# Kernel optimization log

Hardware: AMD Instinct MI355X
Metric: run time of the kernel (lower is better)

## Reference

```python
import jax, jax.numpy as jnp
from jax import lax
import numpy as np

ALPHA = 1.0
GAMMA = 1e-6
KBLK = 64  # codebook block size for the L1 NN search scan


def setup_inputs() -> dict:
    key = jax.random.key(0)
    ks = jax.random.split(key, 6)
    B, T, C, F, D, K = 8, 1024, 32, 256, 128, 512
    return {
        "X": jax.random.normal(ks[0], (B, T, C), jnp.float32),
        "H": jax.random.normal(ks[1], (B, D, T), jnp.float32),
        "M": jax.random.normal(ks[2], (D, K), jnp.float32),
        "Hdec": jax.random.normal(ks[3], (B, T, F), jnp.float32),
        "W": jax.random.normal(ks[4], (C, F), jnp.float32) * 0.05,
        "w_d": jax.random.normal(ks[5], (C,), jnp.float32) * 0.05,
    }


def _memory_loss(H, M):
    # H: [B, D, T], M: [D, K]
    Ht = jnp.transpose(H, (0, 2, 1))            # [B, T, D]
    MT = M.T                                     # [K, D] codewords
    K, D = MT.shape
    nblk = K // KBLK
    blocks = MT.reshape(nblk, KBLK, D)
    bases = jnp.arange(nblk, dtype=jnp.int32) * KBLK

    def step(carry, blk_base):
        best_d, best_i = carry
        blk, base = blk_base
        # L1 distance to this block of codewords: [B, T, KBLK]
        d = jnp.sum(jnp.abs(Ht[:, :, None, :] - blk[None, None, :, :]), axis=-1)
        bd = jnp.min(d, axis=-1)
        bi = jnp.argmin(d, axis=-1).astype(jnp.int32) + base
        upd = bd < best_d  # strict < keeps the first (lowest-index) argmin, as torch does
        return (jnp.where(upd, bd, best_d), jnp.where(upd, bi, best_i)), None

    init = (jnp.full(Ht.shape[:2], jnp.inf, Ht.dtype),
            jnp.zeros(Ht.shape[:2], jnp.int32))
    (_, best_i), _ = lax.scan(step, init, (blocks, bases))

    Zt = MT[best_i]  # [B, T, D] gathered nearest codewords
    sg = lax.stop_gradient
    # sum of per-(b,d) squared L2 norms over T == total squared sum
    diffs = jnp.sum((sg(Ht) - Zt) ** 2) + jnp.sum((Ht - sg(Zt)) ** 2)
    return diffs / float(np.prod(H.shape))


def reference(X, H, M, Hdec, W, w_d):
    # decoder last layer + discriminator head (needed for adaptive weight grads)
    def rec_loss(w):
        Xhat = jnp.einsum('btf,cf->btc', Hdec, w)
        return jnp.mean((Xhat - X) ** 2)

    def d_loss(w):
        Xhat = jnp.einsum('btf,cf->btc', Hdec, w)
        return -jnp.mean(Xhat @ w_d)

    loss_rec = rec_loss(W)
    loss_d = d_loss(W)
    loss_m = _memory_loss(H, M)

    g_rec = jax.grad(rec_loss)(W)
    g_d = jax.grad(d_loss)(W)
    lmbda = lax.stop_gradient(
        jnp.linalg.norm(g_rec) / (jnp.linalg.norm(g_d) + GAMMA))

    return loss_rec + ALPHA * loss_m + lmbda * loss_d
```

## Files before the change

kernel.cpp:

```cpp
#include <hip/hip_runtime.h>
#include <hip/hip_bf16.h>
#include <math.h>

#define N_POS 8192
#define D_DIM 128
#define K_DIM 512
#define C_DIM 32
#define F_DIM 256
#define NKT   4
#define GREC_COLS 8448
#define L2_BLOCKS 388
#define XG_BLOCKS 256
#define NN_BLOCKS 1024
#define GRID_L1   1280

__device__ __forceinline__ void gll16(const float* g, float* l) {
    __builtin_amdgcn_global_load_lds(
        (const __attribute__((address_space(1))) void*)g,
        (__attribute__((address_space(3))) void*)l, 16, 0, 0);
}

__device__ __forceinline__ float block_reduce_256(float v) {
    __shared__ float sbuf[4];
    __syncthreads();
#pragma unroll
    for (int off = 32; off > 0; off >>= 1) v += __shfl_down(v, off);
    const int lane = threadIdx.x & 63;
    const int w    = threadIdx.x >> 6;
    if (lane == 0) sbuf[w] = v;
    __syncthreads();
    return (threadIdx.x == 0) ? (sbuf[0] + sbuf[1] + sbuf[2] + sbuf[3]) : 0.f;
}

__global__ __launch_bounds__(256, 6)
void fused_l1(const float* __restrict__ H, const float* __restrict__ M,
              const float* __restrict__ Hdec, const float* __restrict__ W,
              const float* __restrict__ X, const float* __restrict__ w_d,
              float* __restrict__ MT, float* __restrict__ pd,
              int* __restrict__ pi, float* __restrict__ pp,
              float* __restrict__ accum) {
    __shared__ __align__(16) float smem[5120];
    const int tid = threadIdx.x;

    if (blockIdx.x >= XG_BLOCKS) {
        float* hT = smem;
        float* mT = smem + 1024;
        float* rd = smem;
        int*   ri = (int*)(smem + 1024);

        const int nb    = blockIdx.x - XG_BLOCKS;
        const int ptile = nb >> 2;
        const int ktile = nb & 3;
        const int pos0  = ptile << 5;
        const int b     = pos0 >> 10;
        const int t0    = pos0 & 1023;
        const int k0    = ktile << 7;
        const float* Hb = H + (b << 17) + t0;

        const int wv = tid >> 6;
        const int p4 = (tid & 7) << 2;
        const int q4 = (tid >> 3) << 2;

        const float* hsrc = Hb + (size_t)(tid >> 3) * 1024 + ((tid & 7) << 2);
        const float* msrc = M + (size_t)(tid >> 5) * K_DIM + k0 + ((tid & 31) << 2);
        float* hdstw = hT + (wv << 8);
        float* mdstw = mT + (wv << 8);

        float acc[4][4];
#pragma unroll
        for (int i = 0; i < 4; ++i)
#pragma unroll
            for (int j = 0; j < 4; ++j) acc[i][j] = 0.f;

        auto stage = [&](int ch, int sel) {
            const size_t d0 = (size_t)(ch << 4);
            if (tid < 128)
                gll16(hsrc + (d0 << 10), hdstw + (sel << 9));
#pragma unroll
            for (int p = 0; p < 2; ++p)
                gll16(msrc + (d0 + (size_t)(p << 3)) * K_DIM,
                      mdstw + (sel << 11) + (p << 10));
        };

        stage(0, 0);

        for (int ch = 0; ch < 8; ++ch) {
            __syncthreads();
            if (ch < 7) stage(ch + 1, (ch + 1) & 1);

            const float* hc = hT + ((ch & 1) << 9);
            const float* mc = mT + ((ch & 1) << 11);
#pragma unroll 4
            for (int d = 0; d < 16; ++d) {
                const float4 ha = *(const float4*)(hc + (d << 5) + p4);
                const float4 ma = *(const float4*)(mc + (d << 7) + q4);
                const float hh[4] = {ha.x, ha.y, ha.z, ha.w};
                const float mm[4] = {ma.x, ma.y, ma.z, ma.w};
#pragma unroll
                for (int i = 0; i < 4; ++i)
#pragma unroll
                    for (int j = 0; j < 4; ++j) {
                        const float dv = hh[i] - mm[j];
                        asm("v_add_f32 %0, %0, abs(%1)"
                            : "+v"(acc[i][j]) : "v"(dv));
                    }
            }
        }

        __syncthreads();

        const int kg = tid >> 3;
#pragma unroll
        for (int i = 0; i < 4; ++i) {
            const int pl = p4 + i;
            float bd = acc[i][0];
            int   bj = 0;
#pragma unroll
            for (int j = 1; j < 4; ++j)
                if (acc[i][j] < bd) { bd = acc[i][j]; bj = j; }
            rd[kg * 32 + pl] = bd;
            ri[kg * 32 + pl] = k0 + q4 + bj;
        }
        __syncthreads();

        if (tid < 32) {
            float bd = rd[tid];
            int   bi = ri[tid];
#pragma unroll
            for (int q = 1; q < 32; ++q) {
                const float d = rd[q * 32 + tid];
                const int   k = ri[q * 32 + tid];
                if (d < bd || (d == bd && k < bi)) { bd = d; bi = k; }
            }
            pd[ktile * N_POS + pos0 + tid] = bd;
            pi[ktile * N_POS + pos0 + tid] = bi;
        }
    } else {
        float* El = smem;
        const int xb  = blockIdx.x;
        const int bt0 = xb << 5;

        if (xb < 64) {
            const int d0 = xb << 1;
            const int d  = d0 + (tid >> 7);
            const int k  = (tid & 127) << 2;
#pragma unroll
            for (int j = 0; j < 4; ++j)
                MT[(size_t)(k + j) * D_DIM + d] = M[(size_t)d * K_DIM + k + j];
        }

        const int c  = tid & 31;
        const int rg = tid >> 5;
        const int r0 = bt0 + rg, r1 = r0 + 8, r2 = r0 + 16, r3 = r0 + 24;

        const float* Wc = W + (size_t)c * F_DIM;

        float a0 = 0.f, a1 = 0.f, a2 = 0.f, a3 = 0.f;
#pragma unroll 4
        for (int f0 = 0; f0 < F_DIM; f0 += 4) {
            const float4 w4 = *(const float4*)(Wc + f0);
            const float4 h0 = *(const float4*)(Hdec + (size_t)r0 * F_DIM + f0);
            const float4 h1 = *(const float4*)(Hdec + (size_t)r1 * F_DIM + f0);
            const float4 h2 = *(const float4*)(Hdec + (size_t)r2 * F_DIM + f0);
            const float4 h3 = *(const float4*)(Hdec + (size_t)r3 * F_DIM + f0);
            a0 += h0.x * w4.x + h0.y * w4.y + h0.z * w4.z + h0.w * w4.w;
            a1 += h1.x * w4.x + h1.y * w4.y + h1.z * w4.z + h1.w * w4.w;
            a2 += h2.x * w4.x + h2.y * w4.y + h2.z * w4.z + h2.w * w4.w;
            a3 += h3.x * w4.x + h3.y * w4.y + h3.z * w4.z + h3.w * w4.w;
        }

        const float wd = w_d[c];
        const float e0 = a0 - X[(size_t)r0 * C_DIM + c];
        const float e1 = a1 - X[(size_t)r1 * C_DIM + c];
        const float e2 = a2 - X[(size_t)r2 * C_DIM + c];
        const float e3 = a3 - X[(size_t)r3 * C_DIM + c];
        El[(rg)      * 32 + c] = e0;
        El[(rg + 8)  * 32 + c] = e1;
        El[(rg + 16) * 32 + c] = e2;
        El[(rg + 24) * 32 + c] = e3;
        const float sse = e0 * e0 + e1 * e1 + e2 * e2 + e3 * e3;
        const float dp  = (a0 + a1 + a2 + a3) * wd;
        const float rA = block_reduce_256(sse);
        if (tid == 0) atomicAdd(accum + 0, rA);
        const float rB = block_reduce_256(dp);
        if (tid == 0) atomicAdd(accum + 1, rB);
        __syncthreads();

        const int f = tid;
        const float* hp = Hdec + (size_t)bt0 * F_DIM + f;
        float gacc[C_DIM];
#pragma unroll
        for (int cc = 0; cc < C_DIM; ++cc) gacc[cc] = 0.f;
        float sf = 0.f;
        float hd0 = hp[0];
        float hd1 = hp[F_DIM];
#pragma unroll 1
        for (int i = 0; i < 30; ++i) {
            const float hdn = hp[(size_t)(i + 2) * F_DIM];
            sf += hd0;
#pragma unroll
            for (int c4 = 0; c4 < 8; ++c4) {
                const float4 e4 = *(const float4*)(El + i * 32 + c4 * 4);
                gacc[c4 * 4 + 0] += e4.x * hd0;
                gacc[c4 * 4 + 1] += e4.y * hd0;
                gacc[c4 * 4 + 2] += e4.z * hd0;
                gacc[c4 * 4 + 3] += e4.w * hd0;
            }
            hd0 = hd1; hd1 = hdn;
        }
#pragma unroll
        for (int i = 30; i < 32; ++i) {
            sf += hd0;
#pragma unroll
            for (int c4 = 0; c4 < 8; ++c4) {
                const float4 e4 = *(const float4*)(El + i * 32 + c4 * 4);
                gacc[c4 * 4 + 0] += e4.x * hd0;
                gacc[c4 * 4 + 1] += e4.y * hd0;
                gacc[c4 * 4 + 2] += e4.z * hd0;
                gacc[c4 * 4 + 3] += e4.w * hd0;
            }
            hd0 = hd1;
        }
        float* o = pp + (size_t)xb * GREC_COLS;
#pragma unroll
        for (int cc = 0; cc < C_DIM; ++cc) o[cc * F_DIM + f] = gacc[cc];
        o[8192 + f] = sf;
    }
}

__global__ __launch_bounds__(256)
void fused_l2(const float* __restrict__ H, const float* __restrict__ MT,
              const float* __restrict__ pd, const int* __restrict__ pi,
              const float* __restrict__ pp, const float* __restrict__ w_d,
              float* __restrict__ accum, float* __restrict__ out) {
    const int tid = threadIdx.x;
    if (blockIdx.x < 256) {
        const int bx = blockIdx.x & 31;
        const int by = blockIdx.x >> 5;
        const int pos = bx * 256 + tid;
        const int b = pos >> 10;
        const int t = pos & 1023;

        const int d0 = by * 16;
        const float* Hb = H + (b << 17) + t + (d0 << 10);
        float hv[16];
#pragma unroll
        for (int j = 0; j < 16; ++j) hv[j] = Hb[j << 10];

        float bd = INFINITY;
        int   bi = 0x7fffffff;
#pragma unroll
        for (int p = 0; p < NKT; ++p) {
            const float d = pd[p * N_POS + pos];
            const int   k = pi[p * N_POS + pos];
            if (d < bd || (d == bd && k < bi)) { bd = d; bi = k; }
        }

        const float* z  = MT + (size_t)bi * D_DIM + d0;
        const float4 z0 = *(const float4*)(z);
        const float4 z1 = *(const float4*)(z + 4);
        const float4 z2 = *(const float4*)(z + 8);
        const float4 z3 = *(const float4*)(z + 12);
        float s0 = 0.f, s1 = 0.f, s2 = 0.f, s3 = 0.f;
        float e;
        e = hv[0]  - z0.x; s0 += e * e;
        e = hv[1]  - z0.y; s1 += e * e;
        e = hv[2]  - z0.z; s2 += e * e;
        e = hv[3]  - z0.w; s3 += e * e;
        e = hv[4]  - z1.x; s0 += e * e;
        e = hv[5]  - z1.y; s1 += e * e;
        e = hv[6]  - z1.z; s2 += e * e;
        e = hv[7]  - z1.w; s3 += e * e;
        e = hv[8]  - z2.x; s0 += e * e;
        e = hv[9]  - z2.y; s1 += e * e;
        e = hv[10] - z2.z; s2 += e * e;
        e = hv[11] - z2.w; s3 += e * e;
        e = hv[12] - z3.x; s0 += e * e;
        e = hv[13] - z3.y; s1 += e * e;
        e = hv[14] - z3.z; s2 += e * e;
        e = hv[15] - z3.w; s3 += e * e;
        const float r = block_reduce_256((s0 + s1) + (s2 + s3));
        if (tid == 0) atomicAdd(accum + 2, r);
    } else {
        const int g = blockIdx.x - 256;
        const int col = (g < 128) ? (g * 64 + (tid & 63))
                                  : (8192 + (g - 128) * 64 + (tid & 63));
        const int pc  = tid >> 6;
        const float* base = pp + (size_t)(pc * 64) * GREC_COLS + col;
        float s = 0.f;
#pragma unroll 8
        for (int p = 0; p < 64; ++p) s += base[(size_t)p * GREC_COLS];
        __shared__ float red[4][64];
        red[pc][tid & 63] = s;
        __syncthreads();
        if (tid < 64) {
            const float tot = red[0][tid] + red[1][tid] +
                              red[2][tid] + red[3][tid];
            float v = tot * tot;
#pragma unroll
            for (int off = 32; off > 0; off >>= 1) v += __shfl_down(v, off);
            if (tid == 0)
                atomicAdd(accum + ((g >= 128) ? 4 : 3), v);
        }
    }

    __shared__ int is_last;
    if (tid == 0) {
        __threadfence();
        unsigned int* cnt = (unsigned int*)(accum + 5);
        is_last = (atomicAdd(cnt, 1u) == L2_BLOCKS - 1);
    }
    __syncthreads();
    if (is_last && tid < 64) {
        float wd2 = (tid < C_DIM) ? w_d[tid] * w_d[tid] : 0.f;
#pragma unroll
        for (int off = 32; off > 0; off >>= 1) wd2 += __shfl_down(wd2, off);
        if (tid == 0) {
            __threadfence();
            const float sse_rec = atomicAdd(accum + 0, 0.f);
            const float dsum    = atomicAdd(accum + 1, 0.f);
            const float sse_mem = atomicAdd(accum + 2, 0.f);
            const float g2      = atomicAdd(accum + 3, 0.f);
            const float s2      = atomicAdd(accum + 4, 0.f);
            const float loss_rec = sse_rec / 262144.f;
            const float loss_d   = -dsum / 8192.f;
            const float loss_m   = 2.f * sse_mem / 1048576.f;
            const float ngrec    = (2.f / 262144.f) * sqrtf(g2);
            const float ngd      = sqrtf(wd2 * s2) / 8192.f;
            const float lmbda    = ngrec / (ngd + 1e-6f);
            out[0] = loss_rec + loss_m + lmbda * loss_d;
        }
    }
}

extern "C" void kernel_launch(void* const* d_in, const int* in_sizes, int n_in,
                              void* d_out, int out_size, void* d_ws, size_t ws_size,
                              hipStream_t stream) {
    const float* X    = (const float*)d_in[0];
    const float* H    = (const float*)d_in[1];
    const float* M    = (const float*)d_in[2];
    const float* Hdec = (const float*)d_in[3];
    const float* W    = (const float*)d_in[4];
    const float* w_d  = (const float*)d_in[5];

    float* ws    = (float*)d_ws;
    float* MT    = ws;
    float* accum = ws + 65536;
    float* pd    = ws + 65552;
    int*   pi    = (int*)(ws + 98320);
    float* pp    = ws + 131088;

    hipMemsetAsync(accum, 0, 16 * sizeof(float), stream);
    fused_l1<<<GRID_L1,   256, 0, stream>>>(H, M, Hdec, W, X, w_d,
                                            MT, pd, pi, pp, accum);
    fused_l2<<<L2_BLOCKS, 256, 0, stream>>>(H, MT, pd, pi, pp, w_d,
                                            accum, (float*)d_out);
}
```

Baseline: 122.7 us.

## Enlarge L1 nearest-neighbour tile to 128x128 with 8x8 register micro-tiles

The L1 distance search blocks now cover 128 positions by 128 codewords instead of 32 by 128. Each thread accumulates an 8x8 register tile instead of 4x4, which quarters the number of NN blocks and raises arithmetic intensity per LDS load. Launch bounds drop to 4 waves per SIMD and shared memory shrinks. The cost is higher register pressure, lower occupancy and fewer blocks for the CUs to share.

```diff
diff --git a/kernel.cpp b/kernel.cpp
--- a/kernel.cpp
+++ b/kernel.cpp
@@ -11,8 +11,7 @@
 #define GREC_COLS 8448
 #define L2_BLOCKS 388
 #define XG_BLOCKS 256
-#define NN_BLOCKS 1024
-#define GRID_L1   1280
+#define GRID_L1   512
 
 __device__ __forceinline__ void gll16(const float* g, float* l) {
     __builtin_amdgcn_global_load_lds(
@@ -32,74 +31,72 @@
     return (threadIdx.x == 0) ? (sbuf[0] + sbuf[1] + sbuf[2] + sbuf[3]) : 0.f;
 }
 
-__global__ __launch_bounds__(256, 6)
+__global__ __launch_bounds__(256, 4)
 void fused_l1(const float* __restrict__ H, const float* __restrict__ M,
               const float* __restrict__ Hdec, const float* __restrict__ W,
               const float* __restrict__ X, const float* __restrict__ w_d,
               float* __restrict__ MT, float* __restrict__ pd,
               int* __restrict__ pi, float* __restrict__ pp,
               float* __restrict__ accum) {
-    __shared__ __align__(16) float smem[5120];
+    __shared__ __align__(16) float smem[4096];
     const int tid = threadIdx.x;
 
     if (blockIdx.x >= XG_BLOCKS) {
-        float* hT = smem;
-        float* mT = smem + 1024;
         float* rd = smem;
-        int*   ri = (int*)(smem + 1024);
+        int*   ri = (int*)(smem + 2048);
 
         const int nb    = blockIdx.x - XG_BLOCKS;
         const int ptile = nb >> 2;
         const int ktile = nb & 3;
-        const int pos0  = ptile << 5;
+        const int pos0  = ptile << 7;
         const int b     = pos0 >> 10;
         const int t0    = pos0 & 1023;
         const int k0    = ktile << 7;
         const float* Hb = H + (b << 17) + t0;
 
         const int wv = tid >> 6;
-        const int p4 = (tid & 7) << 2;
-        const int q4 = (tid >> 3) << 2;
-
-        const float* hsrc = Hb + (size_t)(tid >> 3) * 1024 + ((tid & 7) << 2);
+        const int p8 = (tid & 15) << 3;
+        const int q8 = (tid >> 4) << 3;
+
+        const float* hsrc = Hb + (size_t)(tid >> 5) * 1024 + ((tid & 31) << 2);
         const float* msrc = M + (size_t)(tid >> 5) * K_DIM + k0 + ((tid & 31) << 2);
-        float* hdstw = hT + (wv << 8);
-        float* mdstw = mT + (wv << 8);
-
-        float acc[4][4];
-#pragma unroll
-        for (int i = 0; i < 4; ++i)
-#pragma unroll
-            for (int j = 0; j < 4; ++j) acc[i][j] = 0.f;
+        float* hdstw = smem + (wv << 8);
+        float* mdstw = smem + 2048 + (wv << 8);
+
+        float acc[8][8];
+#pragma unroll
+        for (int i = 0; i < 8; ++i)
+#pragma unroll
+            for (int j = 0; j < 8; ++j) acc[i][j] = 0.f;
 
         auto stage = [&](int ch, int sel) {
-            const size_t d0 = (size_t)(ch << 4);
-            if (tid < 128)
-                gll16(hsrc + (d0 << 10), hdstw + (sel << 9));
-#pragma unroll
-            for (int p = 0; p < 2; ++p)
-                gll16(msrc + (d0 + (size_t)(p << 3)) * K_DIM,
-                      mdstw + (sel << 11) + (p << 10));
+            const size_t dd = (size_t)ch << 3;
+            gll16(hsrc + (dd << 10), hdstw + (sel << 10));
+            gll16(msrc + dd * K_DIM, mdstw + (sel << 10));
         };
 
         stage(0, 0);
 
-        for (int ch = 0; ch < 8; ++ch) {
+        for (int ch = 0; ch < 16; ++ch) {
             __syncthreads();
-            if (ch < 7) stage(ch + 1, (ch + 1) & 1);
-
-            const float* hc = hT + ((ch & 1) << 9);
-            const float* mc = mT + ((ch & 1) << 11);
-#pragma unroll 4
-            for (int d = 0; d < 16; ++d) {
-                const float4 ha = *(const float4*)(hc + (d << 5) + p4);
-                const float4 ma = *(const float4*)(mc + (d << 7) + q4);
-                const float hh[4] = {ha.x, ha.y, ha.z, ha.w};
-                const float mm[4] = {ma.x, ma.y, ma.z, ma.w};
-#pragma unroll
-                for (int i = 0; i < 4; ++i)
-#pragma unroll
-                    for (int j = 0; j < 4; ++j) {
+            if (ch < 15) stage(ch + 1, (ch + 1) & 1);
+
+            const float* hc = smem + ((ch & 1) << 10);
+            const float* mc = smem + 2048 + ((ch & 1) << 10);
+#pragma unroll
+            for (int d = 0; d < 8; ++d) {
+                const float4 h0 = *(const float4*)(hc + (d << 7) + p8);
+                const float4 h1 = *(const float4*)(hc + (d << 7) + p8 + 4);
+                const float4 m0 = *(const float4*)(mc + (d << 7) + q8);
+                const float4 m1 = *(const float4*)(mc + (d << 7) + q8 + 4);
+                const float hh[8] = {h0.x, h0.y, h0.z, h0.w,
+                                     h1.x, h1.y, h1.z, h1.w};
+                const float mm[8] = {m0.x, m0.y, m0.z, m0.w,
+                                     m1.x, m1.y, m1.z, m1.w};
+#pragma unroll
+                for (int i = 0; i < 8; ++i)
+#pragma unroll
+                    for (int j = 0; j < 8; ++j) {
                         const float dv = hh[i] - mm[j];
                         asm("v_add_f32 %0, %0, abs(%1)"
                             : "+v"(acc[i][j]) : "v"(dv));
@@ -109,27 +106,27 @@
 
         __syncthreads();
 
-        const int kg = tid >> 3;
-#pragma unroll
-        for (int i = 0; i < 4; ++i) {
-            const int pl = p4 + i;
+        const int kg = tid >> 4;
+#pragma unroll
+        for (int i = 0; i < 8; ++i) {
+            const int pl = p8 + i;
             float bd = acc[i][0];
             int   bj = 0;
 #pragma unroll
-            for (int j = 1; j < 4; ++j)
+            for (int j = 1; j < 8; ++j)
                 if (acc[i][j] < bd) { bd = acc[i][j]; bj = j; }
-            rd[kg * 32 + pl] = bd;
-            ri[kg * 32 + pl] = k0 + q4 + bj;
+            rd[kg * 128 + pl] = bd;
+            ri[kg * 128 + pl] = k0 + q8 + bj;
         }
         __syncthreads();
 
-        if (tid < 32) {
+        if (tid < 128) {
             float bd = rd[tid];
             int   bi = ri[tid];
 #pragma unroll
-            for (int q = 1; q < 32; ++q) {
-                const float d = rd[q * 32 + tid];
-                const int   k = ri[q * 32 + tid];
+            for (int q = 1; q < 16; ++q) {
+                const float d = rd[q * 128 + tid];
+                const int   k = ri[q * 128 + tid];
                 if (d < bd || (d == bd && k < bi)) { bd = d; bi = k; }
             }
             pd[ktile * N_POS + pos0 + tid] = bd;
```

Result: slower. 139.3 us (+13.5%).
